# Kernel tuning notes

Hardware: AMD Instinct MI355X
Metric: run time of the kernel (lower is better)

## Reference

```python
import jax, jax.numpy as jnp
import numpy as np

DIM = 512
NUM_HEADS = 8
HEAD_DIM = DIM // NUM_HEADS
SCALE = HEAD_DIM ** -0.5


def setup_inputs() -> dict:
    key = jax.random.key(0)
    kx, kqw, kqb, kpw, kpb = jax.random.split(key, 5)
    B, N = 2, 4096
    x = jax.random.normal(kx, (B, N, DIM), dtype=jnp.float32)
    # nn.Linear weights stored as [out, in]; init ~ U(-1/sqrt(in), 1/sqrt(in))
    bound = 1.0 / np.sqrt(DIM)
    qkv_w = jax.random.uniform(kqw, (3 * DIM, DIM), minval=-bound, maxval=bound, dtype=jnp.float32)
    qkv_b = jax.random.uniform(kqb, (3 * DIM,), minval=-bound, maxval=bound, dtype=jnp.float32)
    proj_w = jax.random.uniform(kpw, (DIM, DIM), minval=-bound, maxval=bound, dtype=jnp.float32)
    proj_b = jax.random.uniform(kpb, (DIM,), minval=-bound, maxval=bound, dtype=jnp.float32)
    return {"x": x, "qkv_w": qkv_w, "qkv_b": qkv_b, "proj_w": proj_w, "proj_b": proj_b}


def reference(x, qkv_w, qkv_b, proj_w, proj_b):
    B, N, C = x.shape
    # qkv: [B, N, 3C] -> [3, B, H, N, Dh]
    qkv = x @ qkv_w.T + qkv_b
    qkv = qkv.reshape(B, N, 3, NUM_HEADS, HEAD_DIM).transpose(2, 0, 3, 1, 4)
    q, k, v = qkv[0], qkv[1], qkv[2]
    # scores: [B, H, N, N] (materialized, matching the original math)
    attn = jnp.einsum("bhqd,bhkd->bhqk", q, k) * SCALE
    attn = jax.nn.softmax(attn, axis=-1)
    out = jnp.einsum("bhqk,bhkd->bhqd", attn, v)  # [B, H, N, Dh]
    out = out.transpose(0, 2, 1, 3).reshape(B, N, C)
    return out @ proj_w.T + proj_b
```

## Files before the change

### kernel.cpp

```cpp
#include <hip/hip_runtime.h>
#include <hip/hip_bf16.h>
#include <stdint.h>
#include <stddef.h>

typedef __attribute__((ext_vector_type(8))) short short8;
typedef __attribute__((ext_vector_type(4))) float f32x4;
typedef __attribute__((ext_vector_type(16))) float f32x16;

#define MFMA16(a, b, c) __builtin_amdgcn_mfma_f32_16x16x32_bf16((a), (b), (c), 0, 0, 0)
#define MFMA32(a, b, c) __builtin_amdgcn_mfma_f32_32x32x16_bf16((a), (b), (c), 0, 0, 0)

#define QSCALE 0.1803368801111204f

#if __has_builtin(__builtin_amdgcn_exp2f)
#define EXP2(x) __builtin_amdgcn_exp2f(x)
#else
#define EXP2(x) __builtin_exp2f(x)
#endif

__device__ __forceinline__ float b2f(short x) {
    unsigned u = ((unsigned)(unsigned short)x) << 16;
    float f; __builtin_memcpy(&f, &u, 4); return f;
}
__device__ __forceinline__ short f2b(float f) {
    unsigned u; __builtin_memcpy(&u, &f, 4);
    u = (u + 0x7FFFu + ((u >> 16) & 1u)) >> 16;
    return (short)u;
}
__device__ __forceinline__ unsigned pack2(float a, float b) {
    unsigned ua, ub; __builtin_memcpy(&ua, &a, 4); __builtin_memcpy(&ub, &b, 4);
    return __builtin_amdgcn_perm(ub + 0x8000u, ua + 0x8000u, 0x07060302u);
}
__device__ __forceinline__ unsigned cvtpk(float a, float b) {
    unsigned r;
    asm("v_cvt_pk_bf16_f32 %0, %1, %2" : "=v"(r) : "v"(a), "v"(b));
    return r;
}
__device__ __forceinline__ short8 load8f(const float* p) {
    const float4 f0 = *(const float4*)p;
    const float4 f1 = *(const float4*)(p + 4);
    short8 r;
    r[0]=f2b(f0.x); r[1]=f2b(f0.y); r[2]=f2b(f0.z); r[3]=f2b(f0.w);
    r[4]=f2b(f1.x); r[5]=f2b(f1.y); r[6]=f2b(f1.z); r[7]=f2b(f1.w);
    return r;
}

__global__ __launch_bounds__(256) void cvt3(
    const float* __restrict__ s0, short* __restrict__ d0, int n0,
    const float* __restrict__ s1, short* __restrict__ d1, int n1,
    const float* __restrict__ s2, short* __restrict__ d2, int n2)
{
    int i = blockIdx.x * 256 + threadIdx.x;
    if (i < n0) { *(short8*)(d0 + (size_t)i * 8) = load8f(s0 + (size_t)i * 8); return; }
    i -= n0;
    if (i < n1) { *(short8*)(d1 + (size_t)i * 8) = load8f(s1 + (size_t)i * 8); return; }
    i -= n1;
    if (i < n2) { *(short8*)(d2 + (size_t)i * 8) = load8f(s2 + (size_t)i * 8); }
}

__global__ __launch_bounds__(256) void qkv_gemm(
    const short* __restrict__ X, const short* __restrict__ W,
    const float* __restrict__ bias,
    short* __restrict__ Qb, short* __restrict__ Kb, short* __restrict__ Vb)
{
    __shared__ short sT[128][132];

    const int tid  = threadIdx.x;
    const int wv   = tid >> 6;
    const int lane = tid & 63;
    const int l15  = lane & 15;
    const int quad = lane >> 4;
    const int m0   = blockIdx.x * 128 + (wv >> 1) * 64;
    const int sec  = blockIdx.y >> 2;
    const int bis  = blockIdx.y & 3;
    const int nbase = sec * 512 + bis * 128;
    const int j0   = (wv & 1) * 64;

    const f32x4 zero = {0.f, 0.f, 0.f, 0.f};
    f32x4 acc[4][4];
#pragma unroll
    for (int i = 0; i < 4; i++)
#pragma unroll
        for (int j = 0; j < 4; j++) acc[i][j] = zero;

    const short* Arow = X + (size_t)(m0 + l15) * 512 + quad * 8;
    const short* Brow = W + (size_t)(nbase + j0 + l15) * 512 + quad * 8;

    short8 a[4], b[4];
#pragma unroll
    for (int i = 0; i < 4; i++) a[i] = *(const short8*)(Arow + (size_t)i * 16 * 512);
#pragma unroll
    for (int j = 0; j < 4; j++) b[j] = *(const short8*)(Brow + (size_t)j * 16 * 512);

#pragma unroll 2
    for (int k0 = 0; k0 < 512; k0 += 32) {
        const int kn = (k0 + 32 < 512) ? k0 + 32 : 0;
        short8 an[4], bn[4];
#pragma unroll
        for (int i = 0; i < 4; i++) an[i] = *(const short8*)(Arow + (size_t)i * 16 * 512 + kn);
#pragma unroll
        for (int j = 0; j < 4; j++) bn[j] = *(const short8*)(Brow + (size_t)j * 16 * 512 + kn);
#pragma unroll
        for (int i = 0; i < 4; i++)
#pragma unroll
            for (int j = 0; j < 4; j++)
                acc[i][j] = MFMA16(a[i], b[j], acc[i][j]);
#pragma unroll
        for (int i = 0; i < 4; i++) a[i] = an[i];
#pragma unroll
        for (int j = 0; j < 4; j++) b[j] = bn[j];
    }

    if (sec < 2) {
        const float scale = (sec == 0) ? QSCALE : 1.0f;
        short* dst = (sec == 0) ? Qb : Kb;
#pragma unroll
        for (int j = 0; j < 4; j++) {
            const int jcl = j0 + j * 16 + l15;
            const float bs = bias[sec * 512 + bis * 128 + jcl];
#pragma unroll
            for (int i = 0; i < 4; i++) {
                const int s0 = (wv >> 1) * 64 + i * 16 + quad * 4;
#pragma unroll
                for (int r = 0; r < 4; r++)
                    sT[s0 + r][jcl] = f2b((acc[i][j][r] + bs) * scale);
            }
        }
        __syncthreads();

        const int seqlocal = tid & 127;
        const int hl_loc   = tid >> 7;
        const int hl  = bis * 2 + hl_loc;
        const int m   = blockIdx.x * 128 + seqlocal;
        const int bb  = m >> 12, seqg = m & 4095;
        short* drow = dst + ((size_t)(bb * 8 + hl) * 4096 + seqg) * 64;
#pragma unroll
        for (int u = 0; u < 8; u++)
            *(short8*)(drow + u * 8) = *(const short8*)&sT[seqlocal][hl_loc * 64 + u * 8];
    } else {
#pragma unroll
        for (int j = 0; j < 4; j++) {
            const int jcl = j0 + j * 16 + l15;
            const float bs = bias[nbase + jcl];
#pragma unroll
            for (int i = 0; i < 4; i++) {
                uint2 w;
                w.x = pack2(acc[i][j][0] + bs, acc[i][j][1] + bs);
                w.y = pack2(acc[i][j][2] + bs, acc[i][j][3] + bs);
                *(uint2*)&sT[jcl][(wv >> 1) * 64 + i * 16 + quad * 4] = w;
            }
        }
        __syncthreads();

        const int jcl = tid >> 1, half = tid & 1;
        const int hl = (bis * 128 + jcl) >> 6;
        const int d  = jcl & 63;
        const int bb = (blockIdx.x * 128) >> 12;
        const int seq0 = ((blockIdx.x * 128) & 4095) + half * 64;
        short* dst = Vb + ((size_t)(bb * 8 + hl) * 64 + d) * 4096 + seq0;
#pragma unroll
        for (int u = 0; u < 8; u++)
            *(short8*)(dst + u * 8) = *(const short8*)&sT[jcl][half * 64 + u * 8];
    }
}

__global__ __launch_bounds__(512, 4) void flash_attn(
    const short* __restrict__ Q, const short* __restrict__ K,
    const short* __restrict__ V, short* __restrict__ PO0,
    short* __restrict__ PO1, float* __restrict__ lbuf, int niter)
{
    __shared__ short sK[2][128][72];
    __shared__ short sV[2][64][136];

    const int tid  = threadIdx.x;
    const int wv   = tid >> 6;
    const int lane = tid & 63;
    const int l31  = lane & 31;
    const int half = lane >> 5;
    const int bh = blockIdx.y;
    const int b = bh >> 3, h = bh & 7;
    const int qw = blockIdx.x * 256 + wv * 32;
    const int ks = blockIdx.z;
    const int key0 = ks * niter * 128;

    const short* Qb = Q + (size_t)bh * 4096 * 64;
    const short* Kb = K + (size_t)bh * 4096 * 64;
    const short* Vb = V + (size_t)bh * 64 * 4096;

    short8 aq[4];
#pragma unroll
    for (int s = 0; s < 4; s++)
        aq[s] = *(const short8*)(Qb + (size_t)(qw + l31) * 64 + s * 16 + half * 8);

    short8 ones;
#pragma unroll
    for (int j = 0; j < 8; j++) ones[j] = (short)0x3F80;

    f32x16 o0 = {}, o1 = {};
    f32x16 o2 = {};

    const int r0  = tid >> 3;
    const int scb = (tid & 7) * 8;
    const int vb  = (scb & ~12) | ((scb & 8) >> 1);

    short8 pk0, pk1, pv0, pv1;
    pk0 = *(const short8*)(Kb + (size_t)(key0 + r0) * 64 + scb);
    pk1 = *(const short8*)(Kb + (size_t)(key0 + 64 + r0) * 64 + scb);
    pv0 = *(const short8*)(Vb + (size_t)r0 * 4096 + key0 + scb);
    pv1 = *(const short8*)(Vb + (size_t)r0 * 4096 + key0 + 64 + scb);
    *(short8*)&sK[0][r0][scb]      = pk0;
    *(short8*)&sK[0][64 + r0][scb] = pk1;
    *(uint2*)&sV[0][r0][vb]          = ((const uint2*)&pv0)[0];
    *(uint2*)&sV[0][r0][vb + 8]      = ((const uint2*)&pv0)[1];
    *(uint2*)&sV[0][r0][64 + vb]     = ((const uint2*)&pv1)[0];
    *(uint2*)&sV[0][r0][64 + vb + 8] = ((const uint2*)&pv1)[1];
    {
        const int kn = key0 + 128;
        pk0 = *(const short8*)(Kb + (size_t)(kn + r0) * 64 + scb);
        pk1 = *(const short8*)(Kb + (size_t)(kn + 64 + r0) * 64 + scb);
        pv0 = *(const short8*)(Vb + (size_t)r0 * 4096 + kn + scb);
        pv1 = *(const short8*)(Vb + (size_t)r0 * 4096 + kn + 64 + scb);
    }

    for (int kt = 0; kt < niter; ++kt) {
        __syncthreads();

        if (kt + 1 < niter) {
            short (*sKn)[72]  = sK[(kt + 1) & 1];
            short (*sVn)[136] = sV[(kt + 1) & 1];
            *(short8*)&sKn[r0][scb]      = pk0;
            *(short8*)&sKn[64 + r0][scb] = pk1;
            *(uint2*)&sVn[r0][vb]          = ((const uint2*)&pv0)[0];
            *(uint2*)&sVn[r0][vb + 8]      = ((const uint2*)&pv0)[1];
            *(uint2*)&sVn[r0][64 + vb]     = ((const uint2*)&pv1)[0];
            *(uint2*)&sVn[r0][64 + vb + 8] = ((const uint2*)&pv1)[1];
        }
        if (kt + 2 < niter) {
            const int kn = key0 + (kt + 2) * 128;
            pk0 = *(const short8*)(Kb + (size_t)(kn + r0) * 64 + scb);
            pk1 = *(const short8*)(Kb + (size_t)(kn + 64 + r0) * 64 + scb);
            pv0 = *(const short8*)(Vb + (size_t)r0 * 4096 + kn + scb);
            pv1 = *(const short8*)(Vb + (size_t)r0 * 4096 + kn + 64 + scb);
        }

        const short (*sKc)[72]  = sK[kt & 1];
        const short (*sVc)[136] = sV[kt & 1];

#pragma unroll
        for (int i = 0; i < 4; i++) {
            const int c = (i + wv) & 3;
            f32x16 ST = {};
            __builtin_amdgcn_s_setprio(1);
#pragma unroll
            for (int s = 0; s < 4; s++) {
                const short8 bk = *(const short8*)&sKc[c * 32 + l31][s * 16 + half * 8];
                ST = MFMA32(bk, aq[s], ST);
            }
            __builtin_amdgcn_s_setprio(0);
            float e[16];
#pragma unroll
            for (int r = 0; r < 16; r++) e[r] = EXP2(ST[r]);
            uint4 w0 = { cvtpk(e[0], e[1]),   cvtpk(e[2], e[3]),
                         cvtpk(e[4], e[5]),   cvtpk(e[6], e[7]) };
            uint4 w1 = { cvtpk(e[8], e[9]),   cvtpk(e[10], e[11]),
                         cvtpk(e[12], e[13]), cvtpk(e[14], e[15]) };
            const short8 bp0 = *(const short8*)&w0;
            const short8 bp1 = *(const short8*)&w1;

            __builtin_amdgcn_s_setprio(1);
            const short8 bv00 = *(const short8*)&sVc[l31][(2 * c) * 16 + half * 8];
            const short8 bv01 = *(const short8*)&sVc[32 + l31][(2 * c) * 16 + half * 8];
            o0 = MFMA32(bv00, bp0, o0);
            o1 = MFMA32(bv01, bp0, o1);
            o2 = MFMA32(ones, bp0, o2);
            const short8 bv10 = *(const short8*)&sVc[l31][(2 * c + 1) * 16 + half * 8];
            const short8 bv11 = *(const short8*)&sVc[32 + l31][(2 * c + 1) * 16 + half * 8];
            o0 = MFMA32(bv10, bp1, o0);
            o1 = MFMA32(bv11, bp1, o1);
            o2 = MFMA32(ones, bp1, o2);
            __builtin_amdgcn_s_setprio(0);
        }
    }

    const float lsum = o2[0];
    const float inv = 1.f / fmaxf(lsum, 1e-30f);

    short* PO = (ks == 0) ? PO0 : PO1;
#pragma unroll
    for (int q = 0; q < 4; q++) {
        uint2 w0, w1;
        w0.x = pack2(o0[4 * q + 0] * inv, o0[4 * q + 1] * inv);
        w0.y = pack2(o0[4 * q + 2] * inv, o0[4 * q + 3] * inv);
        w1.x = pack2(o1[4 * q + 0] * inv, o1[4 * q + 1] * inv);
        w1.y = pack2(o1[4 * q + 2] * inv, o1[4 * q + 3] * inv);
        const size_t rowoff = ((size_t)b * 4096 + qw + l31) * 512;
        const int col = h * 64 + q * 8 + half * 4;
        *(uint2*)(PO + rowoff + col) = w0;
        *(uint2*)(PO + rowoff + col + 32) = w1;
    }
    if (half == 0)
        lbuf[((size_t)ks * 16 + bh) * 4096 + qw + l31] = lsum;
}

__global__ __launch_bounds__(256) void combine(
    const short* __restrict__ PO0, const short* __restrict__ PO1,
    short* __restrict__ attn, const float* __restrict__ L)
{
    const int i = blockIdx.x * 256 + threadIdx.x;
    const size_t flat = (size_t)i * 8;
    const int col = (int)(flat & 511);
    const int q   = (int)((flat >> 9) & 4095);
    const int b   = (int)(flat >> 21);
    const int bh  = b * 8 + (col >> 6);
    const float l0 = L[(size_t)bh * 4096 + q];
    const float l1 = L[(size_t)65536 + (size_t)bh * 4096 + q];
    const float inv = 1.f / (l0 + l1);
    const float w0 = l0 * inv, w1 = l1 * inv;
    const short8 a = *(const short8*)(PO0 + flat);
    const short8 c = *(const short8*)(PO1 + flat);
    short8 r;
#pragma unroll
    for (int k = 0; k < 8; k += 2) {
        const unsigned p = pack2(w0 * b2f(a[k]) + w1 * b2f(c[k]),
                                 w0 * b2f(a[k + 1]) + w1 * b2f(c[k + 1]));
        r[k]     = (short)(p & 0xFFFF);
        r[k + 1] = (short)(p >> 16);
    }
    *(short8*)(attn + flat) = r;
}

__global__ __launch_bounds__(256) void proj_gemm(
    const short* __restrict__ A, const short* __restrict__ W,
    const float* __restrict__ bias, float* __restrict__ dst)
{
    const int tid  = threadIdx.x;
    const int wv   = tid >> 6;
    const int lane = tid & 63;
    const int l15  = lane & 15;
    const int quad = lane >> 4;
    const int m0 = blockIdx.x * 64;
    const int n0 = blockIdx.y * 128 + wv * 32;

    const f32x4 zero = {0.f, 0.f, 0.f, 0.f};
    f32x4 acc[4][2];
#pragma unroll
    for (int i = 0; i < 4; i++)
#pragma unroll
        for (int j = 0; j < 2; j++) acc[i][j] = zero;

    const short* Arow = A + (size_t)(m0 + l15) * 512 + quad * 8;
    const short* Brow = W + (size_t)(n0 + l15) * 512 + quad * 8;

    short8 a[4], b[2];
#pragma unroll
    for (int i = 0; i < 4; i++) a[i] = *(const short8*)(Arow + (size_t)i * 16 * 512);
#pragma unroll
    for (int j = 0; j < 2; j++) b[j] = *(const short8*)(Brow + (size_t)j * 16 * 512);

#pragma unroll 2
    for (int k0 = 0; k0 < 512; k0 += 32) {
        const int kn = (k0 + 32 < 512) ? k0 + 32 : 0;
        short8 an[4], bn[2];
#pragma unroll
        for (int i = 0; i < 4; i++) an[i] = *(const short8*)(Arow + (size_t)i * 16 * 512 + kn);
#pragma unroll
        for (int j = 0; j < 2; j++) bn[j] = *(const short8*)(Brow + (size_t)j * 16 * 512 + kn);
#pragma unroll
        for (int i = 0; i < 4; i++)
#pragma unroll
            for (int j = 0; j < 2; j++)
                acc[i][j] = MFMA16(b[j], a[i], acc[i][j]);
#pragma unroll
        for (int i = 0; i < 4; i++) a[i] = an[i];
#pragma unroll
        for (int j = 0; j < 2; j++) b[j] = bn[j];
    }

#pragma unroll
    for (int i = 0; i < 4; i++) {
        const int m = m0 + i * 16 + l15;
#pragma unroll
        for (int j = 0; j < 2; j++) {
            const int n = n0 + j * 16 + quad * 4;
            const float4 bs = *(const float4*)(bias + n);
            float4 o;
            o.x = acc[i][j][0] + bs.x;
            o.y = acc[i][j][1] + bs.y;
            o.z = acc[i][j][2] + bs.z;
            o.w = acc[i][j][3] + bs.w;
            *(float4*)(dst + (size_t)m * 512 + n) = o;
        }
    }
}

extern "C" void kernel_launch(void* const* d_in, const int* in_sizes, int n_in,
                              void* d_out, int out_size, void* d_ws, size_t ws_size,
                              hipStream_t stream)
{
    const float* x      = (const float*)d_in[0];
    const float* qkv_w  = (const float*)d_in[1];
    const float* qkv_b  = (const float*)d_in[2];
    const float* proj_w = (const float*)d_in[3];
    const float* proj_b = (const float*)d_in[4];

    const size_t MB = 1024 * 1024;
    short* xb   = (short*)d_out;
    short* wb   = (short*)d_out + 4 * MB;
    short* PO0  = (short*)d_out;
    short* PO1  = (short*)d_out + 4 * MB;
    float* out  = (float*)d_out;

    short* Qf = (short*)d_ws;
    short* Kf = Qf + (size_t)16 * 4096 * 64;
    short* Vf = Kf + (size_t)16 * 4096 * 64;
    short* attn = Qf;
    float* lbuf = (float*)((char*)d_ws + 24 * MB);
    short* pwb  = (short*)((char*)d_ws + 24 * MB + 512 * 1024);

    cvt3<<<2560, 256, 0, stream>>>(x, xb, 524288, qkv_w, wb, 98304, proj_w, pwb, 32768);
    qkv_gemm<<<dim3(64, 12), 256, 0, stream>>>(xb, wb, qkv_b, Qf, Kf, Vf);
    flash_attn<<<dim3(16, 16, 2), 512, 0, stream>>>(Qf, Kf, Vf, PO0, PO1, lbuf, 16);
    combine<<<2048, 256, 0, stream>>>(PO0, PO1, attn, lbuf);
    proj_gemm<<<dim3(128, 4), 256, 0, stream>>>(attn, pwb, proj_b, out);
}
```

Before: 235.4 us.

## Fuse fp32-to-bf16 conversion into GEMMs and split-K combine into projection

Removes the standalone cvt3 conversion kernel by having qkv_gemm and the projection read fp32 inputs and weights directly, converting them to bf16 in registers with v_cvt_pk_bf16_f32. It also removes the combine kernel by merging the two split-K attention partials, weighted by their softmax sums, inside the projection GEMM's A-operand load. Buffers are reassigned between the output and workspace to match. This drops two launches and the intermediate bf16 round trips through memory. In exchange the GEMMs read twice the bytes per operand, redo the conversion in every tile that touches the same data, and lose the explicit register double-buffered prefetch, which may expose load latency.

```diff
diff --git a/kernel.cpp b/kernel.cpp
--- a/kernel.cpp
+++ b/kernel.cpp
@@ -36,30 +36,24 @@
     asm("v_cvt_pk_bf16_f32 %0, %1, %2" : "=v"(r) : "v"(a), "v"(b));
     return r;
 }
-__device__ __forceinline__ short8 load8f(const float* p) {
+__device__ __forceinline__ short8 cvt8f(const float* p) {
     const float4 f0 = *(const float4*)p;
     const float4 f1 = *(const float4*)(p + 4);
-    short8 r;
-    r[0]=f2b(f0.x); r[1]=f2b(f0.y); r[2]=f2b(f0.z); r[3]=f2b(f0.w);
-    r[4]=f2b(f1.x); r[5]=f2b(f1.y); r[6]=f2b(f1.z); r[7]=f2b(f1.w);
-    return r;
-}
-
-__global__ __launch_bounds__(256) void cvt3(
-    const float* __restrict__ s0, short* __restrict__ d0, int n0,
-    const float* __restrict__ s1, short* __restrict__ d1, int n1,
-    const float* __restrict__ s2, short* __restrict__ d2, int n2)
-{
-    int i = blockIdx.x * 256 + threadIdx.x;
-    if (i < n0) { *(short8*)(d0 + (size_t)i * 8) = load8f(s0 + (size_t)i * 8); return; }
-    i -= n0;
-    if (i < n1) { *(short8*)(d1 + (size_t)i * 8) = load8f(s1 + (size_t)i * 8); return; }
-    i -= n1;
-    if (i < n2) { *(short8*)(d2 + (size_t)i * 8) = load8f(s2 + (size_t)i * 8); }
+    uint4 u = { cvtpk(f0.x, f0.y), cvtpk(f0.z, f0.w),
+                cvtpk(f1.x, f1.y), cvtpk(f1.z, f1.w) };
+    return *(short8*)&u;
+}
+__device__ __forceinline__ short8 comb8(short8 a0, short8 a1, float w0, float w1) {
+    float f[8];
+#pragma unroll
+    for (int e = 0; e < 8; e++) f[e] = w0 * b2f(a0[e]) + w1 * b2f(a1[e]);
+    uint4 u = { cvtpk(f[0], f[1]), cvtpk(f[2], f[3]),
+                cvtpk(f[4], f[5]), cvtpk(f[6], f[7]) };
+    return *(short8*)&u;
 }
 
 __global__ __launch_bounds__(256) void qkv_gemm(
-    const short* __restrict__ X, const short* __restrict__ W,
+    const float* __restrict__ X, const float* __restrict__ W,
     const float* __restrict__ bias,
     short* __restrict__ Qb, short* __restrict__ Kb, short* __restrict__ Vb)
 {
@@ -83,32 +77,21 @@
 #pragma unroll
         for (int j = 0; j < 4; j++) acc[i][j] = zero;
 
-    const short* Arow = X + (size_t)(m0 + l15) * 512 + quad * 8;
-    const short* Brow = W + (size_t)(nbase + j0 + l15) * 512 + quad * 8;
-
-    short8 a[4], b[4];
-#pragma unroll
-    for (int i = 0; i < 4; i++) a[i] = *(const short8*)(Arow + (size_t)i * 16 * 512);
-#pragma unroll
-    for (int j = 0; j < 4; j++) b[j] = *(const short8*)(Brow + (size_t)j * 16 * 512);
+    const float* Arow = X + (size_t)(m0 + l15) * 512 + quad * 8;
+    const float* Brow = W + (size_t)(nbase + j0 + l15) * 512 + quad * 8;
 
 #pragma unroll 2
     for (int k0 = 0; k0 < 512; k0 += 32) {
-        const int kn = (k0 + 32 < 512) ? k0 + 32 : 0;
-        short8 an[4], bn[4];
-#pragma unroll
-        for (int i = 0; i < 4; i++) an[i] = *(const short8*)(Arow + (size_t)i * 16 * 512 + kn);
-#pragma unroll
-        for (int j = 0; j < 4; j++) bn[j] = *(const short8*)(Brow + (size_t)j * 16 * 512 + kn);
+        short8 a[4], b[4];
+#pragma unroll
+        for (int i = 0; i < 4; i++) a[i] = cvt8f(Arow + (size_t)i * 16 * 512 + k0);
+#pragma unroll
+        for (int j = 0; j < 4; j++) b[j] = cvt8f(Brow + (size_t)j * 16 * 512 + k0);
 #pragma unroll
         for (int i = 0; i < 4; i++)
 #pragma unroll
             for (int j = 0; j < 4; j++)
                 acc[i][j] = MFMA16(a[i], b[j], acc[i][j]);
-#pragma unroll
-        for (int i = 0; i < 4; i++) a[i] = an[i];
-#pragma unroll
-        for (int j = 0; j < 4; j++) b[j] = bn[j];
     }
 
     if (sec < 2) {
@@ -302,35 +285,9 @@
         lbuf[((size_t)ks * 16 + bh) * 4096 + qw + l31] = lsum;
 }
 
-__global__ __launch_bounds__(256) void combine(
+__global__ __launch_bounds__(256) void proj_fused(
     const short* __restrict__ PO0, const short* __restrict__ PO1,
-    short* __restrict__ attn, const float* __restrict__ L)
-{
-    const int i = blockIdx.x * 256 + threadIdx.x;
-    const size_t flat = (size_t)i * 8;
-    const int col = (int)(flat & 511);
-    const int q   = (int)((flat >> 9) & 4095);
-    const int b   = (int)(flat >> 21);
-    const int bh  = b * 8 + (col >> 6);
-    const float l0 = L[(size_t)bh * 4096 + q];
-    const float l1 = L[(size_t)65536 + (size_t)bh * 4096 + q];
-    const float inv = 1.f / (l0 + l1);
-    const float w0 = l0 * inv, w1 = l1 * inv;
-    const short8 a = *(const short8*)(PO0 + flat);
-    const short8 c = *(const short8*)(PO1 + flat);
-    short8 r;
-#pragma unroll
-    for (int k = 0; k < 8; k += 2) {
-        const unsigned p = pack2(w0 * b2f(a[k]) + w1 * b2f(c[k]),
-                                 w0 * b2f(a[k + 1]) + w1 * b2f(c[k + 1]));
-        r[k]     = (short)(p & 0xFFFF);
-        r[k + 1] = (short)(p >> 16);
-    }
-    *(short8*)(attn + flat) = r;
-}
-
-__global__ __launch_bounds__(256) void proj_gemm(
-    const short* __restrict__ A, const short* __restrict__ W,
+    const float* __restrict__ L, const float* __restrict__ W,
     const float* __restrict__ bias, float* __restrict__ dst)
 {
     const int tid  = threadIdx.x;
@@ -340,6 +297,7 @@
     const int quad = lane >> 4;
     const int m0 = blockIdx.x * 64;
     const int n0 = blockIdx.y * 128 + wv * 32;
+    const int bb = m0 >> 12;
 
     const f32x4 zero = {0.f, 0.f, 0.f, 0.f};
     f32x4 acc[4][2];
@@ -348,32 +306,39 @@
 #pragma unroll
         for (int j = 0; j < 2; j++) acc[i][j] = zero;
 
-    const short* Arow = A + (size_t)(m0 + l15) * 512 + quad * 8;
-    const short* Brow = W + (size_t)(n0 + l15) * 512 + quad * 8;
-
-    short8 a[4], b[2];
-#pragma unroll
-    for (int i = 0; i < 4; i++) a[i] = *(const short8*)(Arow + (size_t)i * 16 * 512);
-#pragma unroll
-    for (int j = 0; j < 2; j++) b[j] = *(const short8*)(Brow + (size_t)j * 16 * 512);
-
-#pragma unroll 2
-    for (int k0 = 0; k0 < 512; k0 += 32) {
-        const int kn = (k0 + 32 < 512) ? k0 + 32 : 0;
-        short8 an[4], bn[2];
-#pragma unroll
-        for (int i = 0; i < 4; i++) an[i] = *(const short8*)(Arow + (size_t)i * 16 * 512 + kn);
-#pragma unroll
-        for (int j = 0; j < 2; j++) bn[j] = *(const short8*)(Brow + (size_t)j * 16 * 512 + kn);
-#pragma unroll
-        for (int i = 0; i < 4; i++)
-#pragma unroll
-            for (int j = 0; j < 2; j++)
-                acc[i][j] = MFMA16(b[j], a[i], acc[i][j]);
-#pragma unroll
-        for (int i = 0; i < 4; i++) a[i] = an[i];
-#pragma unroll
-        for (int j = 0; j < 2; j++) b[j] = bn[j];
+    const short* A0row = PO0 + (size_t)(m0 + l15) * 512 + quad * 8;
+    const short* A1row = PO1 + (size_t)(m0 + l15) * 512 + quad * 8;
+    const float* Brow  = W + (size_t)(n0 + l15) * 512 + quad * 8;
+
+    for (int h = 0; h < 8; ++h) {
+        float w0v[4], w1v[4];
+#pragma unroll
+        for (int i = 0; i < 4; i++) {
+            const int q = (m0 + i * 16 + l15) & 4095;
+            const size_t off = (size_t)(bb * 8 + h) * 4096 + q;
+            const float l0 = L[off];
+            const float l1 = L[65536 + off];
+            const float inv = 1.f / (l0 + l1);
+            w0v[i] = l0 * inv; w1v[i] = l1 * inv;
+        }
+#pragma unroll
+        for (int kk = 0; kk < 2; ++kk) {
+            const int k0 = h * 64 + kk * 32;
+            short8 a[4], b[2];
+#pragma unroll
+            for (int i = 0; i < 4; i++) {
+                const short8 a0 = *(const short8*)(A0row + (size_t)i * 16 * 512 + k0);
+                const short8 a1 = *(const short8*)(A1row + (size_t)i * 16 * 512 + k0);
+                a[i] = comb8(a0, a1, w0v[i], w1v[i]);
+            }
+#pragma unroll
+            for (int j = 0; j < 2; j++) b[j] = cvt8f(Brow + (size_t)j * 16 * 512 + k0);
+#pragma unroll
+            for (int i = 0; i < 4; i++)
+#pragma unroll
+                for (int j = 0; j < 2; j++)
+                    acc[i][j] = MFMA16(b[j], a[i], acc[i][j]);
+        }
     }
 
 #pragma unroll
@@ -404,22 +369,16 @@
     const float* proj_b = (const float*)d_in[4];
 
     const size_t MB = 1024 * 1024;
-    short* xb   = (short*)d_out;
-    short* wb   = (short*)d_out + 4 * MB;
-    short* PO0  = (short*)d_out;
-    short* PO1  = (short*)d_out + 4 * MB;
-    float* out  = (float*)d_out;
-
-    short* Qf = (short*)d_ws;
-    short* Kf = Qf + (size_t)16 * 4096 * 64;
-    short* Vf = Kf + (size_t)16 * 4096 * 64;
-    short* attn = Qf;
+    short* Kf  = (short*)d_out;
+    short* Vf  = (short*)d_out + 4 * MB;
+    float* out = (float*)d_out;
+
+    short* Qf   = (short*)d_ws;
+    short* PO0  = (short*)((char*)d_ws + 8 * MB);
+    short* PO1  = (short*)((char*)d_ws + 16 * MB);
     float* lbuf = (float*)((char*)d_ws + 24 * MB);
-    short* pwb  = (short*)((char*)d_ws + 24 * MB + 512 * 1024);
-
-    cvt3<<<2560, 256, 0, stream>>>(x, xb, 524288, qkv_w, wb, 98304, proj_w, pwb, 32768);
-    qkv_gemm<<<dim3(64, 12), 256, 0, stream>>>(xb, wb, qkv_b, Qf, Kf, Vf);
+
+    qkv_gemm<<<dim3(64, 12), 256, 0, stream>>>(x, qkv_w, qkv_b, Qf, Kf, Vf);
     flash_attn<<<dim3(16, 16, 2), 512, 0, stream>>>(Qf, Kf, Vf, PO0, PO1, lbuf, 16);
-    combine<<<2048, 256, 0, stream>>>(PO0, PO1, attn, lbuf);
-    proj_gemm<<<dim3(128, 4), 256, 0, stream>>>(attn, pwb, proj_b, out);
-}
+    proj_fused<<<dim3(128, 4), 256, 0, stream>>>(PO0, PO1, lbuf, proj_w, proj_b, out);
+}
```

After: 288.4 us. +22.5%, slower.
